# Kernel optimization log

Measured on AMD Instinct MI355X. Metric: run time of the kernel, lower is better.

## Reference

```python
import jax, jax.numpy as jnp
import numpy as np

EMBED_DIM = 1024
N_HEADS = 16
HEAD_DIM = EMBED_DIM // N_HEADS
B, S = 4, 2048


def _rope_tables(seq_len, dim):
    inv_freq = 1.0 / (10000.0 ** (jnp.arange(0, dim, 2, dtype=jnp.float32) / dim))
    freqs = jnp.arange(seq_len, dtype=jnp.float32)[:, None] * inv_freq[None, :]  # [S, dim/2]
    return jnp.cos(freqs), jnp.sin(freqs)


def _apply_rope(x, cos, sin):
    # x: [B, H, S, D]; interleaved-pair complex rotation
    x2 = x.reshape(*x.shape[:-1], HEAD_DIM // 2, 2)
    x0, x1 = x2[..., 0], x2[..., 1]
    c = cos[None, None, :, :]
    s = sin[None, None, :, :]
    r0 = x0 * c - x1 * s
    r1 = x0 * s + x1 * c
    return jnp.stack([r0, r1], axis=-1).reshape(x.shape)


def setup_inputs() -> dict:
    key = jax.random.key(0)
    ks = jax.random.split(key, 8)
    sc = 0.02
    return {
        "query": jax.random.normal(ks[0], (B, S, EMBED_DIM), jnp.float32),
        "key": jax.random.normal(ks[1], (B, S, EMBED_DIM), jnp.float32),
        "value": jax.random.normal(ks[2], (B, S, EMBED_DIM), jnp.float32),
        "Wq": jax.random.normal(ks[3], (EMBED_DIM, EMBED_DIM), jnp.float32) * sc,
        "Wk": jax.random.normal(ks[4], (EMBED_DIM, EMBED_DIM), jnp.float32) * sc,
        "Wv": jax.random.normal(ks[5], (EMBED_DIM, EMBED_DIM), jnp.float32) * sc,
        "Wo": jax.random.normal(ks[6], (EMBED_DIM, EMBED_DIM), jnp.float32) * sc,
        "bo": jnp.zeros((EMBED_DIM,), jnp.float32),
    }


def reference(query, key, value, Wq, Wk, Wv, Wo, bo):
    b, s, _ = query.shape
    # torch nn.Linear: y = x @ W.T
    Q = (query @ Wq.T).reshape(b, s, N_HEADS, HEAD_DIM).transpose(0, 2, 1, 3)
    K = (key @ Wk.T).reshape(b, s, N_HEADS, HEAD_DIM).transpose(0, 2, 1, 3)
    V = (value @ Wv.T).reshape(b, s, N_HEADS, HEAD_DIM).transpose(0, 2, 1, 3)
    cos, sin = _rope_tables(s, HEAD_DIM)
    Q = _apply_rope(Q, cos, sin)
    K = _apply_rope(K, cos, sin)
    scores = jnp.einsum("bhqd,bhkd->bhqk", Q, K) / jnp.sqrt(jnp.float32(HEAD_DIM))
    attn = jax.nn.softmax(scores, axis=-1)
    out = jnp.einsum("bhqk,bhkd->bhqd", attn, V)
    out = out.transpose(0, 2, 1, 3).reshape(b, s, EMBED_DIM)
    return out @ Wo.T + bo
```

## Files before the change

kernel.cpp:

```cpp
#include <hip/hip_runtime.h>
#include <math.h>

typedef __attribute__((ext_vector_type(4))) float f32x4;
typedef __attribute__((ext_vector_type(16))) float f32x16;
typedef __attribute__((ext_vector_type(8))) __bf16 bf16x8;
typedef __attribute__((ext_vector_type(4))) unsigned int u32x4;
typedef __attribute__((ext_vector_type(4))) unsigned short u16x4;

#define DEVI __device__ __forceinline__

constexpr size_t WS_WB  = 0;
constexpr size_t WS_COS = 4ull * 1024 * 1024 * 2;
constexpr size_t WS_SIN = WS_COS + 2048 * 32 * 4;
constexpr size_t WS_QH  = WS_SIN + 2048 * 32 * 4;
constexpr size_t WS_KH  = WS_QH + 64ull * 2048 * 64 * 2;
constexpr size_t WS_VT  = WS_KH + 64ull * 2048 * 64 * 2;
constexpr size_t WS_AO  = WS_VT + 64ull * 64 * 2048 * 2;

DEVI unsigned short f2bf(float x) {
  union { float f; unsigned int u; } v; v.f = x;
  unsigned int r = v.u + 0x7fffu + ((v.u >> 16) & 1u);
  return (unsigned short)(r >> 16);
}

DEVI unsigned cvtpk(float a, float b) {
  union { __bf16 h[2]; unsigned u; } x;
  x.h[0] = (__bf16)a; x.h[1] = (__bf16)b;
  return x.u;
}

DEVI void ld_lds16(const void* g, void* l) {
  __builtin_amdgcn_global_load_lds((const __attribute__((address_space(1))) void*)g,
                                   (__attribute__((address_space(3))) void*)l, 16, 0, 0);
}

__global__ __launch_bounds__(256) void cvt_w(const float* __restrict__ w0,
                                             const float* __restrict__ w1,
                                             const float* __restrict__ w2,
                                             const float* __restrict__ w3,
                                             unsigned short* __restrict__ out) {
  const float* w = blockIdx.y == 0 ? w0 : blockIdx.y == 1 ? w1 : blockIdx.y == 2 ? w2 : w3;
  int i = (blockIdx.x * 256 + threadIdx.x) * 4;
  f32x4 v = *(const f32x4*)(w + i);
  u16x4 o;
  o.x = f2bf(v.x); o.y = f2bf(v.y); o.z = f2bf(v.z); o.w = f2bf(v.w);
  *(u16x4*)(out + (size_t)blockIdx.y * 1048576 + i) = o;
}

__global__ __launch_bounds__(256) void rope_tab(float* __restrict__ cosT,
                                                float* __restrict__ sinT) {
  int idx = blockIdx.x * 256 + threadIdx.x;
  int s = idx >> 5, i = idx & 31;
  double ang = (double)s * pow(10000.0, -(double)i / 32.0);
  cosT[idx] = (float)cos(ang);
  sinT[idx] = (float)sin(ang);
}

template <int EPI, bool AF32>
__global__ __launch_bounds__(256) void gemm_mha(const void* __restrict__ Av,
                                                const unsigned short* __restrict__ W,
                                                void* __restrict__ outp,
                                                const float* __restrict__ cosT,
                                                const float* __restrict__ sinT,
                                                const float* __restrict__ bo) {
  __shared__ __align__(16) char AsRaw[AF32 ? 16384 : 8192];
  __shared__ __align__(16) unsigned short Bs[128 * 32];

  const int tid = threadIdx.x;
  const int lane = tid & 63;
  const int wave = tid >> 6;
  const int flat = blockIdx.x;
  const int wgid = (flat & 7) * 64 + (flat >> 3);
  const int m0 = (wgid >> 3) * 128;
  const int n0 = (wgid & 7) * 128;
  const int wm = (wave >> 1) * 64;
  const int wn = (wave & 1) * 64;
  const int hi2 = lane >> 4;

  const float* Af = (const float*)Av;
  const unsigned short* Ab = (const unsigned short*)Av;
  float* AsF = (float*)AsRaw;
  unsigned short* Asb = (unsigned short*)AsRaw;

  f32x4 acc[4][4] = {};

  for (int kt = 0; kt < 32; ++kt) {
    const int k0 = kt * 32;
    if constexpr (AF32) {
#pragma unroll
      for (int i = 0; i < 4; ++i) {
        int g = i * 256 + tid;
        int row = g >> 3, u = g & 7;
        ld_lds16(Af + (size_t)(m0 + row) * 1024 + k0 + ((u ^ (row & 7)) << 2),
                 AsF + ((i * 256 + wave * 64) << 2));
      }
    } else {
#pragma unroll
      for (int i = 0; i < 2; ++i) {
        int g = i * 256 + tid;
        int row = g >> 2, u = g & 3;
        ld_lds16(Ab + (size_t)(m0 + row) * 1024 + k0 + ((u ^ ((row >> 1) & 3)) << 3),
                 Asb + ((i * 256 + wave * 64) << 3));
      }
    }
#pragma unroll
    for (int i = 0; i < 2; ++i) {
      int g = i * 256 + tid;
      int row = g >> 2, u = g & 3;
      ld_lds16(W + (size_t)(n0 + row) * 1024 + k0 + ((u ^ ((row >> 1) & 3)) << 3),
               Bs + ((i * 256 + wave * 64) << 3));
    }
    __syncthreads();

    bf16x8 af[4], bfr[4];
#pragma unroll
    for (int x = 0; x < 4; ++x) {
      if constexpr (AF32) {
        int row = wm + x * 16 + (lane & 15);
        int swz = row & 7;
        f32x4 a0 = *(const f32x4*)(AsF + row * 32 + (((hi2 * 2) ^ swz) << 2));
        f32x4 a1 = *(const f32x4*)(AsF + row * 32 + (((hi2 * 2 + 1) ^ swz) << 2));
        union { u32x4 u; bf16x8 v; } f;
        f.u.x = cvtpk(a0.x, a0.y); f.u.y = cvtpk(a0.z, a0.w);
        f.u.z = cvtpk(a1.x, a1.y); f.u.w = cvtpk(a1.z, a1.w);
        af[x] = f.v;
      } else {
        int row = wm + x * 16 + (lane & 15);
        af[x] = *(const bf16x8*)(Asb + row * 32 + ((hi2 ^ ((row >> 1) & 3)) << 3));
      }
      int brow = wn + x * 16 + (lane & 15);
      bfr[x] = *(const bf16x8*)(Bs + brow * 32 + ((hi2 ^ ((brow >> 1) & 3)) << 3));
    }
#pragma unroll
    for (int mi = 0; mi < 4; ++mi)
#pragma unroll
      for (int ni = 0; ni < 4; ++ni)
        acc[mi][ni] = __builtin_amdgcn_mfma_f32_16x16x32_bf16(af[mi], bfr[ni], acc[mi][ni], 0, 0, 0);
    __syncthreads();
  }

  const int b = m0 >> 11;
  const int sbase = (m0 & 2047) + wm + ((lane >> 4) << 2);

  if constexpr (EPI == 0 || EPI == 1) {
    unsigned short* dst = (unsigned short*)outp;
#pragma unroll
    for (int ni = 0; ni < 4; ++ni) {
      int n = n0 + wn + ni * 16 + (lane & 15);
      int h = n >> 6, d = n & 63, fi = d >> 1;
      size_t base = (size_t)(b * 16 + h) * 131072 + d;
#pragma unroll
      for (int mi = 0; mi < 4; ++mi) {
#pragma unroll
        for (int r = 0; r < 4; ++r) {
          int s = sbase + mi * 16 + r;
          float v = acc[mi][ni][r];
          float p = __shfl_xor(v, 1);
          float c = cosT[(s << 5) + fi], sn = sinT[(s << 5) + fi];
          float ov = (d & 1) ? (p * sn + v * c) : (v * c - p * sn);
          if (EPI == 0) ov *= 0.18033688011112042f;
          dst[base + (size_t)s * 64] = f2bf(ov);
        }
      }
    }
  } else if constexpr (EPI == 2) {
    unsigned short* dst = (unsigned short*)outp;
#pragma unroll
    for (int ni = 0; ni < 4; ++ni) {
      int n = n0 + wn + ni * 16 + (lane & 15);
      int h = n >> 6, d = n & 63;
#pragma unroll
      for (int mi = 0; mi < 4; ++mi) {
        u16x4 pk;
        pk.x = f2bf(acc[mi][ni][0]); pk.y = f2bf(acc[mi][ni][1]);
        pk.z = f2bf(acc[mi][ni][2]); pk.w = f2bf(acc[mi][ni][3]);
        int s = sbase + mi * 16;
        *(u16x4*)(dst + ((size_t)(b * 16 + h) * 64 + d) * 2048 + s) = pk;
      }
    }
  } else {
    float* dst = (float*)outp;
#pragma unroll
    for (int ni = 0; ni < 4; ++ni) {
      int n = n0 + wn + ni * 16 + (lane & 15);
      float bias = bo[n];
#pragma unroll
      for (int mi = 0; mi < 4; ++mi)
#pragma unroll
        for (int r = 0; r < 4; ++r) {
          int m = m0 + wm + mi * 16 + ((lane >> 4) << 2) + r;
          dst[(size_t)m * 1024 + n] = acc[mi][ni][r] + bias;
        }
    }
  }
}

DEVI float tile_sm(f32x16& s0, f32x16& s1, bf16x8* pa) {
  float a0 = 0.f, a1 = 0.f, a2 = 0.f, a3 = 0.f;
#pragma unroll
  for (int r = 0; r < 16; r += 4) {
    s0[r] = __builtin_amdgcn_exp2f(s0[r]);         a0 += s0[r];
    s0[r + 1] = __builtin_amdgcn_exp2f(s0[r + 1]); a1 += s0[r + 1];
    s0[r + 2] = __builtin_amdgcn_exp2f(s0[r + 2]); a2 += s0[r + 2];
    s0[r + 3] = __builtin_amdgcn_exp2f(s0[r + 3]); a3 += s0[r + 3];
  }
#pragma unroll
  for (int r = 0; r < 16; r += 4) {
    s1[r] = __builtin_amdgcn_exp2f(s1[r]);         a0 += s1[r];
    s1[r + 1] = __builtin_amdgcn_exp2f(s1[r + 1]); a1 += s1[r + 1];
    s1[r + 2] = __builtin_amdgcn_exp2f(s1[r + 2]); a2 += s1[r + 2];
    s1[r + 3] = __builtin_amdgcn_exp2f(s1[r + 3]); a3 += s1[r + 3];
  }
#pragma unroll
  for (int blk = 0; blk < 2; ++blk) {
    const f32x16& s = blk ? s1 : s0;
#pragma unroll
    for (int half = 0; half < 2; ++half) {
      int o = half * 8;
      unsigned u0 = cvtpk(s[o + 0], s[o + 1]);
      unsigned u1 = cvtpk(s[o + 2], s[o + 3]);
      unsigned u2 = cvtpk(s[o + 4], s[o + 5]);
      unsigned u3 = cvtpk(s[o + 6], s[o + 7]);
      auto r02 = __builtin_amdgcn_permlane32_swap(u0, u2, false, false);
      auto r13 = __builtin_amdgcn_permlane32_swap(u1, u3, false, false);
      union { u32x4 u; bf16x8 v; } f;
      f.u.x = r02[0]; f.u.y = r13[0]; f.u.z = r02[1]; f.u.w = r13[1];
      pa[blk * 2 + half] = f.v;
    }
  }
  return (a0 + a1) + (a2 + a3);
}

__global__ __launch_bounds__(256, 2) void attn_kernel(const unsigned short* __restrict__ Qh,
                                                      const unsigned short* __restrict__ Kh,
                                                      const unsigned short* __restrict__ Vt,
                                                      unsigned short* __restrict__ AOb) {
  __shared__ __align__(16) unsigned short SM[4][4096];

  const int tid = threadIdx.x, lane = tid & 63, wave = tid >> 6;
  const int lid = blockIdx.x;
  const int xcd = lid & 7, slot = lid >> 3;
  const int bh = xcd * 8 + (slot >> 3);
  const int qb = slot & 7;
  const int q0 = qb * 256 + wave * 64;
  const int lq = lane & 31, hi = lane >> 5;

  const unsigned short* Qgb = Qh + (size_t)bh * 131072;
  const unsigned short* Kgb = Kh + (size_t)bh * 131072;
  const unsigned short* Vgb = Vt + (size_t)bh * 131072;

  bf16x8 qfa[4], qfb[4];
#pragma unroll
  for (int st = 0; st < 4; ++st) {
    qfa[st] = *(const bf16x8*)(Qgb + (size_t)(q0 + lq) * 64 + st * 16 + hi * 8);
    qfb[st] = *(const bf16x8*)(Qgb + (size_t)(q0 + 32 + lq) * 64 + st * 16 + hi * 8);
  }

  const int r0 = wave * 8 + (lane >> 3);
  const int u0 = lane & 7;
  const int sw = (u0 ^ (r0 & 7)) << 3;
  const unsigned short* kp0 = Kgb + r0 * 64 + sw;
  const unsigned short* kp1 = Kgb + (32 + r0) * 64 + sw;
  const unsigned short* vp0 = Vgb + (size_t)r0 * 2048 + sw;
  const unsigned short* vp1 = Vgb + (size_t)(32 + r0) * 2048 + sw;
  const int d0 = wave * 512, d1 = 2048 + wave * 512;

  auto stage = [&](int buf, int kt) {
    unsigned short* Kd = SM[buf * 2];
    unsigned short* Vd = SM[buf * 2 + 1];
    ld_lds16(kp0 + kt * 4096, Kd + d0);
    ld_lds16(kp1 + kt * 4096, Kd + d1);
    ld_lds16(vp0 + kt * 64, Vd + d0);
    ld_lds16(vp1 + kt * 64, Vd + d1);
  };
  auto frag = [&](const unsigned short* base, int row, int c) -> bf16x8 {
    return *(const bf16x8*)(base + row * 64 + (((c ^ (row & 7)) << 3)));
  };

  f32x16 o0a = {}, o1a = {}, o0b = {}, o1b = {};
  float lsA = 0.f, lsB = 0.f;

  stage(0, 0);

  for (int kt = 0; kt < 32; ++kt) {
    if (kt < 31) {
      stage((kt + 1) & 1, kt + 1);
      asm volatile("s_waitcnt vmcnt(4)" ::: "memory");
    } else {
      asm volatile("s_waitcnt vmcnt(0)" ::: "memory");
    }
    __builtin_amdgcn_s_barrier();
    const unsigned short* Kc = SM[(kt & 1) * 2];
    const unsigned short* Vc = SM[(kt & 1) * 2 + 1];

    f32x16 s0a = {}, s1a = {}, s0b = {}, s1b = {};
#pragma unroll
    for (int st = 0; st < 4; ++st) {
      bf16x8 k0 = frag(Kc, lq, st * 2 + hi);
      bf16x8 k1 = frag(Kc, 32 + lq, st * 2 + hi);
      s0a = __builtin_amdgcn_mfma_f32_32x32x16_bf16(k0, qfa[st], s0a, 0, 0, 0);
      s1a = __builtin_amdgcn_mfma_f32_32x32x16_bf16(k1, qfa[st], s1a, 0, 0, 0);
      s0b = __builtin_amdgcn_mfma_f32_32x32x16_bf16(k0, qfb[st], s0b, 0, 0, 0);
      s1b = __builtin_amdgcn_mfma_f32_32x32x16_bf16(k1, qfb[st], s1b, 0, 0, 0);
    }

    bf16x8 paA[4], paB[4];
    lsA += tile_sm(s0a, s1a, paA);
    lsB += tile_sm(s0b, s1b, paB);

#pragma unroll
    for (int kc = 0; kc < 4; ++kc) {
      bf16x8 v0 = frag(Vc, lq, kc * 2 + hi);
      bf16x8 v1 = frag(Vc, 32 + lq, kc * 2 + hi);
      o0a = __builtin_amdgcn_mfma_f32_32x32x16_bf16(paA[kc], v0, o0a, 0, 0, 0);
      o1a = __builtin_amdgcn_mfma_f32_32x32x16_bf16(paA[kc], v1, o1a, 0, 0, 0);
      o0b = __builtin_amdgcn_mfma_f32_32x32x16_bf16(paB[kc], v0, o0b, 0, 0, 0);
      o1b = __builtin_amdgcn_mfma_f32_32x32x16_bf16(paB[kc], v1, o1b, 0, 0, 0);
    }
    __builtin_amdgcn_s_barrier();
  }

  lsA += __shfl_xor(lsA, 32);
  lsB += __shfl_xor(lsB, 32);
  const int b = bh >> 4, h = bh & 15;
#pragma unroll
  for (int r = 0; r < 16; ++r) {
    int row = (r & 3) + 8 * (r >> 2) + 4 * hi;
    float ia = 1.0f / __shfl(lsA, row);
    float ib = 1.0f / __shfl(lsB, row);
    unsigned short* da = AOb + (size_t)(b * 2048 + q0 + row) * 1024 + h * 64;
    unsigned short* db = AOb + (size_t)(b * 2048 + q0 + 32 + row) * 1024 + h * 64;
    da[lq] = f2bf(o0a[r] * ia);
    da[32 + lq] = f2bf(o1a[r] * ia);
    db[lq] = f2bf(o0b[r] * ib);
    db[32 + lq] = f2bf(o1b[r] * ib);
  }
}

extern "C" void kernel_launch(void* const* d_in, const int* in_sizes, int n_in,
                              void* d_out, int out_size, void* d_ws, size_t ws_size,
                              hipStream_t stream) {
  const float* query = (const float*)d_in[0];
  const float* key = (const float*)d_in[1];
  const float* value = (const float*)d_in[2];
  const float* Wq = (const float*)d_in[3];
  const float* Wk = (const float*)d_in[4];
  const float* Wv = (const float*)d_in[5];
  const float* Wo = (const float*)d_in[6];
  const float* bo = (const float*)d_in[7];

  char* ws = (char*)d_ws;
  unsigned short* Wb = (unsigned short*)(ws + WS_WB);
  float* cosT = (float*)(ws + WS_COS);
  float* sinT = (float*)(ws + WS_SIN);
  unsigned short* Qh = (unsigned short*)(ws + WS_QH);
  unsigned short* Kh = (unsigned short*)(ws + WS_KH);
  unsigned short* Vt = (unsigned short*)(ws + WS_VT);
  unsigned short* AOb = (unsigned short*)(ws + WS_AO);

  cvt_w<<<dim3(1024, 4), 256, 0, stream>>>(Wq, Wk, Wv, Wo, Wb);
  rope_tab<<<256, 256, 0, stream>>>(cosT, sinT);
  gemm_mha<0, true><<<512, 256, 0, stream>>>(query, Wb, Qh, cosT, sinT, nullptr);
  gemm_mha<1, true><<<512, 256, 0, stream>>>(key, Wb + 1048576, Kh, cosT, sinT, nullptr);
  gemm_mha<2, true><<<512, 256, 0, stream>>>(value, Wb + 2097152, Vt, cosT, sinT, nullptr);
  attn_kernel<<<512, 256, 0, stream>>>(Qh, Kh, Vt, AOb);
  gemm_mha<3, false><<<512, 256, 0, stream>>>(AOb, Wb + 3145728, d_out, cosT, sinT, bo);
}
```

Baseline: 231.9 us.

## Double-buffer GEMM LDS tiles and restructure attention prefetch with one barrier per tile

The projection GEMM gets two LDS buffers for A and B, so the next k-tile's global-to-LDS loads are issued before computing on the current tile. This replaces two __syncthreads per iteration with a single waitcnt plus barrier. The attention loop now waits for the prefetch at the end of each iteration instead of the start, and hoists all K/V fragment reads from LDS ahead of the MFMAs. It also raises wave priority around the MFMA blocks. The costs are double the LDS footprint in the GEMM, which may lower occupancy, and more registers in attention from holding all fragments.

```diff
diff --git a/kernel.cpp b/kernel.cpp
--- a/kernel.cpp
+++ b/kernel.cpp
@@ -63,8 +63,8 @@
                                                 const float* __restrict__ cosT,
                                                 const float* __restrict__ sinT,
                                                 const float* __restrict__ bo) {
-  __shared__ __align__(16) char AsRaw[AF32 ? 16384 : 8192];
-  __shared__ __align__(16) unsigned short Bs[128 * 32];
+  __shared__ __align__(16) char AsRaw[2][AF32 ? 16384 : 8192];
+  __shared__ __align__(16) unsigned short Bs[2][4096];
 
   const int tid = threadIdx.x;
   const int lane = tid & 63;
@@ -79,14 +79,13 @@
 
   const float* Af = (const float*)Av;
   const unsigned short* Ab = (const unsigned short*)Av;
-  float* AsF = (float*)AsRaw;
-  unsigned short* Asb = (unsigned short*)AsRaw;
 
   f32x4 acc[4][4] = {};
 
-  for (int kt = 0; kt < 32; ++kt) {
+  auto stage = [&](int buf, int kt) {
     const int k0 = kt * 32;
     if constexpr (AF32) {
+      float* AsF = (float*)AsRaw[buf];
 #pragma unroll
       for (int i = 0; i < 4; ++i) {
         int g = i * 256 + tid;
@@ -95,6 +94,7 @@
                  AsF + ((i * 256 + wave * 64) << 2));
       }
     } else {
+      unsigned short* Asb = (unsigned short*)AsRaw[buf];
 #pragma unroll
       for (int i = 0; i < 2; ++i) {
         int g = i * 256 + tid;
@@ -108,15 +108,25 @@
       int g = i * 256 + tid;
       int row = g >> 2, u = g & 3;
       ld_lds16(W + (size_t)(n0 + row) * 1024 + k0 + ((u ^ ((row >> 1) & 3)) << 3),
-               Bs + ((i * 256 + wave * 64) << 3));
-    }
-    __syncthreads();
-
+               Bs[buf] + ((i * 256 + wave * 64) << 3));
+    }
+  };
+
+  stage(0, 0);
+  asm volatile("s_waitcnt vmcnt(0)" ::: "memory");
+  __builtin_amdgcn_s_barrier();
+
+  for (int kt = 0; kt < 32; ++kt) {
+    const int cur = kt & 1;
+    if (kt < 31) stage(cur ^ 1, kt + 1);
+
+    const float* AsF = (const float*)AsRaw[cur];
+    const unsigned short* Asb = (const unsigned short*)AsRaw[cur];
     bf16x8 af[4], bfr[4];
 #pragma unroll
     for (int x = 0; x < 4; ++x) {
+      int row = wm + x * 16 + (lane & 15);
       if constexpr (AF32) {
-        int row = wm + x * 16 + (lane & 15);
         int swz = row & 7;
         f32x4 a0 = *(const f32x4*)(AsF + row * 32 + (((hi2 * 2) ^ swz) << 2));
         f32x4 a1 = *(const f32x4*)(AsF + row * 32 + (((hi2 * 2 + 1) ^ swz) << 2));
@@ -125,18 +135,21 @@
         f.u.z = cvtpk(a1.x, a1.y); f.u.w = cvtpk(a1.z, a1.w);
         af[x] = f.v;
       } else {
-        int row = wm + x * 16 + (lane & 15);
         af[x] = *(const bf16x8*)(Asb + row * 32 + ((hi2 ^ ((row >> 1) & 3)) << 3));
       }
       int brow = wn + x * 16 + (lane & 15);
-      bfr[x] = *(const bf16x8*)(Bs + brow * 32 + ((hi2 ^ ((brow >> 1) & 3)) << 3));
+      bfr[x] = *(const bf16x8*)(Bs[cur] + brow * 32 + ((hi2 ^ ((brow >> 1) & 3)) << 3));
     }
 #pragma unroll
     for (int mi = 0; mi < 4; ++mi)
 #pragma unroll
       for (int ni = 0; ni < 4; ++ni)
         acc[mi][ni] = __builtin_amdgcn_mfma_f32_16x16x32_bf16(af[mi], bfr[ni], acc[mi][ni], 0, 0, 0);
-    __syncthreads();
+
+    if (kt < 31) {
+      asm volatile("s_waitcnt vmcnt(0)" ::: "memory");
+      __builtin_amdgcn_s_barrier();
+    }
   }
 
   const int b = m0 >> 11;
@@ -281,43 +294,53 @@
   float lsA = 0.f, lsB = 0.f;
 
   stage(0, 0);
+  asm volatile("s_waitcnt vmcnt(0)" ::: "memory");
+  __builtin_amdgcn_s_barrier();
 
   for (int kt = 0; kt < 32; ++kt) {
-    if (kt < 31) {
-      stage((kt + 1) & 1, kt + 1);
-      asm volatile("s_waitcnt vmcnt(4)" ::: "memory");
-    } else {
-      asm volatile("s_waitcnt vmcnt(0)" ::: "memory");
-    }
-    __builtin_amdgcn_s_barrier();
-    const unsigned short* Kc = SM[(kt & 1) * 2];
-    const unsigned short* Vc = SM[(kt & 1) * 2 + 1];
+    const int cur = kt & 1;
+    if (kt < 31) stage(cur ^ 1, kt + 1);
+    const unsigned short* Kc = SM[cur * 2];
+    const unsigned short* Vc = SM[cur * 2 + 1];
+
+    bf16x8 kf0[4], kf1[4], vf0[4], vf1[4];
+#pragma unroll
+    for (int st = 0; st < 4; ++st) {
+      kf0[st] = frag(Kc, lq, st * 2 + hi);
+      kf1[st] = frag(Kc, 32 + lq, st * 2 + hi);
+      vf0[st] = frag(Vc, lq, st * 2 + hi);
+      vf1[st] = frag(Vc, 32 + lq, st * 2 + hi);
+    }
 
     f32x16 s0a = {}, s1a = {}, s0b = {}, s1b = {};
+    __builtin_amdgcn_s_setprio(1);
 #pragma unroll
     for (int st = 0; st < 4; ++st) {
-      bf16x8 k0 = frag(Kc, lq, st * 2 + hi);
-      bf16x8 k1 = frag(Kc, 32 + lq, st * 2 + hi);
-      s0a = __builtin_amdgcn_mfma_f32_32x32x16_bf16(k0, qfa[st], s0a, 0, 0, 0);
-      s1a = __builtin_amdgcn_mfma_f32_32x32x16_bf16(k1, qfa[st], s1a, 0, 0, 0);
-      s0b = __builtin_amdgcn_mfma_f32_32x32x16_bf16(k0, qfb[st], s0b, 0, 0, 0);
-      s1b = __builtin_amdgcn_mfma_f32_32x32x16_bf16(k1, qfb[st], s1b, 0, 0, 0);
-    }
+      s0a = __builtin_amdgcn_mfma_f32_32x32x16_bf16(kf0[st], qfa[st], s0a, 0, 0, 0);
+      s1a = __builtin_amdgcn_mfma_f32_32x32x16_bf16(kf1[st], qfa[st], s1a, 0, 0, 0);
+      s0b = __builtin_amdgcn_mfma_f32_32x32x16_bf16(kf0[st], qfb[st], s0b, 0, 0, 0);
+      s1b = __builtin_amdgcn_mfma_f32_32x32x16_bf16(kf1[st], qfb[st], s1b, 0, 0, 0);
+    }
+    __builtin_amdgcn_s_setprio(0);
 
     bf16x8 paA[4], paB[4];
     lsA += tile_sm(s0a, s1a, paA);
     lsB += tile_sm(s0b, s1b, paB);
 
+    __builtin_amdgcn_s_setprio(1);
 #pragma unroll
     for (int kc = 0; kc < 4; ++kc) {
-      bf16x8 v0 = frag(Vc, lq, kc * 2 + hi);
-      bf16x8 v1 = frag(Vc, 32 + lq, kc * 2 + hi);
-      o0a = __builtin_amdgcn_mfma_f32_32x32x16_bf16(paA[kc], v0, o0a, 0, 0, 0);
-      o1a = __builtin_amdgcn_mfma_f32_32x32x16_bf16(paA[kc], v1, o1a, 0, 0, 0);
-      o0b = __builtin_amdgcn_mfma_f32_32x32x16_bf16(paB[kc], v0, o0b, 0, 0, 0);
-      o1b = __builtin_amdgcn_mfma_f32_32x32x16_bf16(paB[kc], v1, o1b, 0, 0, 0);
-    }
-    __builtin_amdgcn_s_barrier();
+      o0a = __builtin_amdgcn_mfma_f32_32x32x16_bf16(paA[kc], vf0[kc], o0a, 0, 0, 0);
+      o1a = __builtin_amdgcn_mfma_f32_32x32x16_bf16(paA[kc], vf1[kc], o1a, 0, 0, 0);
+      o0b = __builtin_amdgcn_mfma_f32_32x32x16_bf16(paB[kc], vf0[kc], o0b, 0, 0, 0);
+      o1b = __builtin_amdgcn_mfma_f32_32x32x16_bf16(paB[kc], vf1[kc], o1b, 0, 0, 0);
+    }
+    __builtin_amdgcn_s_setprio(0);
+
+    if (kt < 31) {
+      asm volatile("s_waitcnt vmcnt(0)" ::: "memory");
+      __builtin_amdgcn_s_barrier();
+    }
   }
 
   lsA += __shfl_xor(lsA, 32);
```

Result: slower. 270.3 us (+16.6%).
